# Performance work log

Hardware: AMD Instinct MI355X
Metric: run time of the kernel (lower is better)

The kernel has to match this reference:

```python
import jax, jax.numpy as jnp
import numpy as np

H = 32      # n_heads
KV = 8      # n_kv_heads
HD = 64     # head_dim = dim // n_heads


def setup_inputs() -> dict:
    key = jax.random.key(0)
    ks = jax.random.split(key, 8)
    B, S, D = 4, 1024, 2048
    x = jax.random.normal(ks[0], (B, S, D), dtype=jnp.float32)
    # RoPE tables stored as cos/sin parts of the complex freqs_cis (seqlen, head_dim//2)
    pos = jnp.arange(S, dtype=jnp.float32)[:, None]
    inv = 1.0 / (10000.0 ** (jnp.arange(0, HD, 2, dtype=jnp.float32) / HD))[None, :]
    ang = pos * inv                          # (S, HD//2)
    freqs_cos = jnp.cos(ang)
    freqs_sin = jnp.sin(ang)
    # additive causal mask (S, S): 0 on/below diagonal, -inf above
    mask = jnp.where(jnp.tril(jnp.ones((S, S), dtype=bool)), 0.0, -jnp.inf).astype(jnp.float32)
    sc = 0.02
    wq = jax.random.normal(ks[1], (H * HD, D), dtype=jnp.float32) * sc
    wk = jax.random.normal(ks[2], (KV * HD, D), dtype=jnp.float32) * sc
    wv = jax.random.normal(ks[3], (KV * HD, D), dtype=jnp.float32) * sc
    wo = jax.random.normal(ks[4], (D, D), dtype=jnp.float32) * sc
    return {"x": x, "freqs_cos": freqs_cos, "freqs_sin": freqs_sin, "mask": mask,
            "wq": wq, "wk": wk, "wv": wv, "wo": wo}


def _rope(t, cos, sin):
    # t: (B, S, nh, HD). Faithful to source: rotation is indexed by x.shape[2]
    # (the HEAD axis, due to pre-transpose call), broadcast over sequence.
    nh = t.shape[2]
    c = cos[:nh][None, None, :, :]           # (1,1,nh,HD//2)
    s = sin[:nh][None, None, :, :]
    tr = t.reshape(*t.shape[:-1], HD // 2, 2)
    t0, t1 = tr[..., 0], tr[..., 1]
    o0 = t0 * c - t1 * s
    o1 = t0 * s + t1 * c
    return jnp.stack([o0, o1], axis=-1).reshape(t.shape)


def reference(x, freqs_cos, freqs_sin, mask, wq, wk, wv, wo):
    B, S, D = x.shape
    xq = (x @ wq.T).reshape(B, S, H, HD)
    xk = (x @ wk.T).reshape(B, S, KV, HD)
    xv = (x @ wv.T).reshape(B, S, KV, HD)
    xq = _rope(xq, freqs_cos, freqs_sin)
    xk = _rope(xk, freqs_cos, freqs_sin)
    rep = H // KV
    xk = jnp.repeat(xk, rep, axis=2)         # GQA repeat_interleave on head axis
    xv = jnp.repeat(xv, rep, axis=2)
    q = xq.transpose(0, 2, 1, 3)             # (B,H,S,HD)
    k = xk.transpose(0, 2, 1, 3)
    v = xv.transpose(0, 2, 1, 3)
    scores = jnp.einsum('bhqd,bhkd->bhqk', q, k) / np.sqrt(HD).astype(np.float32)
    scores = scores + mask[None, None, :, :]
    p = jax.nn.softmax(scores.astype(jnp.float32), axis=-1).astype(q.dtype)
    out = jnp.einsum('bhqk,bhkd->bhqd', p, v)
    out = out.transpose(0, 2, 1, 3).reshape(B, S, H * HD)
    return out @ wo.T
```

## Files before the change

kernel.cpp:

```cpp
#include <hip/hip_runtime.h>
#include <hip/hip_bf16.h>

constexpr int kB  = 4;
constexpr int kS  = 1024;
constexpr int kD  = 2048;
constexpr int kH  = 32;
constexpr int kKV = 8;
constexpr int kHD = 64;
constexpr int kM  = kB * kS;
constexpr int kNT = kS / 64;

constexpr float kNegBig = -30000.0f;
constexpr float kC = 0.125f * 1.44269504f;
constexpr float kDeferThr = 40.0f;

typedef __attribute__((ext_vector_type(8))) short short8;
typedef __attribute__((ext_vector_type(4))) float floatx4;

static __device__ __forceinline__ short f2bf(float f) {
    unsigned int u = __builtin_bit_cast(unsigned int, f);
    unsigned int lsb = (u >> 16) & 1u;
    u += 0x7fffu + lsb;
    return (short)(u >> 16);
}
static __device__ __forceinline__ short f2bf_fast(float f) {
    unsigned int u = __builtin_bit_cast(unsigned int, f);
    return (short)((u + 0x8000u) >> 16);
}

static __device__ __forceinline__ void load_lds16(const short* g, short* l) {
    __builtin_amdgcn_global_load_lds(
        (const __attribute__((address_space(1))) unsigned int*)g,
        (__attribute__((address_space(3))) unsigned int*)l, 16, 0, 0);
}

__global__ void cast_f2b(const float* __restrict__ in, short* __restrict__ outp, int n4) {
    int gid = blockIdx.x * blockDim.x + threadIdx.x;
    if (gid >= n4) return;
    float4 v = ((const float4*)in)[gid];
    short4 o;
    o.x = f2bf(v.x); o.y = f2bf(v.y); o.z = f2bf(v.z); o.w = f2bf(v.w);
    ((short4*)outp)[gid] = o;
}

__global__ void cast4_f2b(const float* __restrict__ a, const float* __restrict__ b,
                          const float* __restrict__ c, const float* __restrict__ d,
                          short* __restrict__ oa, short* __restrict__ ob,
                          short* __restrict__ oc, short* __restrict__ od,
                          int na4, int nb4, int nc4, int nd4) {
    int gid = blockIdx.x * blockDim.x + threadIdx.x;
    const float* src; short* dst; int idx;
    if (gid < na4)                    { src = a; dst = oa; idx = gid; }
    else if (gid < na4 + nb4)         { src = b; dst = ob; idx = gid - na4; }
    else if (gid < na4 + nb4 + nc4)   { src = c; dst = oc; idx = gid - na4 - nb4; }
    else if (gid < na4+nb4+nc4+nd4)   { src = d; dst = od; idx = gid - na4 - nb4 - nc4; }
    else return;
    float4 v = ((const float4*)src)[idx];
    short4 o;
    o.x = f2bf(v.x); o.y = f2bf(v.y); o.z = f2bf(v.z); o.w = f2bf(v.w);
    ((short4*)dst)[idx] = o;
}

template <typename OT, int ROPE>
__global__ __launch_bounds__(256) void gemm_bt_lds(const short* __restrict__ A,
                                                   const short* __restrict__ Bm,
                                                   OT* __restrict__ C,
                                                   int M, int N, int K,
                                                   const float* __restrict__ cosb,
                                                   const float* __restrict__ sinb,
                                                   short* __restrict__ Vt,
                                                   const short* __restrict__ B2,
                                                   short* __restrict__ Kout) {
    __shared__ short As[128 * 32];
    __shared__ short Bs[128 * 32];

    int tid  = threadIdx.x;
    int wave = tid >> 6, lane = tid & 63;
    int quad = lane >> 4, l16 = lane & 15;
    int wm = wave >> 1, wn = wave & 1;

    int nwg  = gridDim.x * gridDim.y;
    int orig = blockIdx.y * gridDim.x + blockIdx.x;
    int wg   = orig;
    if ((nwg & 7) == 0) {
        int cpx = nwg >> 3;
        wg = (orig & 7) * cpx + (orig >> 3);
    }
    int bx = wg % gridDim.x, by = wg / gridDim.x;
    int m0 = by * 128, n0 = bx * 128;

    const short* Bblk;
    if constexpr (ROPE == 3)
        Bblk = (n0 < 2048) ? Bm + (long)n0 * K : B2 + (long)(n0 - 2048) * K;
    else
        Bblk = Bm + (long)n0 * K;

    floatx4 acc[4][4];
    for (int i = 0; i < 4; i++)
        for (int j = 0; j < 4; j++) acc[i][j] = (floatx4){0.f, 0.f, 0.f, 0.f};

    int srow = lane >> 2;
    int skc  = (lane & 3) * 8;

    for (int k0 = 0; k0 < K; k0 += 32) {
        __syncthreads();
        for (int i = 0; i < 2; i++) {
            int r16 = wave * 32 + i * 16;
            load_lds16(A + (long)(m0 + r16 + srow) * K + k0 + skc, &As[r16 * 32]);
            load_lds16(Bblk + (long)(r16 + srow) * K + k0 + skc, &Bs[r16 * 32]);
        }
        __syncthreads();

        short8 af[4], bfr[4];
        for (int i = 0; i < 4; i++)
            af[i] = *(const short8*)&As[(wm * 64 + i * 16 + l16) * 32 + quad * 8];
        for (int j = 0; j < 4; j++)
            bfr[j] = *(const short8*)&Bs[(wn * 64 + j * 16 + l16) * 32 + quad * 8];
        for (int i = 0; i < 4; i++)
            for (int j = 0; j < 4; j++)
                acc[i][j] = __builtin_amdgcn_mfma_f32_16x16x32_bf16(
                    af[i], bfr[j], acc[i][j], 0, 0, 0);
    }

    if constexpr (ROPE == 3) {
        for (int j = 0; j < 4; j++) {
            int col = n0 + wn * 64 + j * 16 + l16;
            if (col >= 2560) {
                int cv = col - 2560;
                for (int i = 0; i < 4; i++) {
                    int row0 = m0 + wm * 64 + i * 16 + quad * 4;
                    short4 o;
                    o.x = f2bf(acc[i][j][0]);
                    o.y = f2bf(acc[i][j][1]);
                    o.z = f2bf(acc[i][j][2]);
                    o.w = f2bf(acc[i][j][3]);
                    *(short4*)&Vt[(long)cv * M + row0] = o;
                }
            } else {
                bool isK = col >= 2048;
                int hh = isK ? ((col - 2048) >> 6) : (col >> 6);
                int ii = (col & 63) >> 1;
                float c = cosb[hh * 32 + ii];
                float s = sinb[hh * 32 + ii];
                for (int i = 0; i < 4; i++) {
                    for (int r = 0; r < 4; r++) {
                        int row = m0 + wm * 64 + i * 16 + quad * 4 + r;
                        float v = acc[i][j][r];
                        float p = __shfl_xor(v, 1);
                        v = (col & 1) ? (p * s + v * c)
                                      : (v * c - p * s);
                        if (isK)
                            Kout[(long)row * 1024 + (col - 2048)] = f2bf(v);
                        else
                            ((short*)C)[(long)row * 2048 + col] = f2bf(v);
                    }
                }
            }
        }
    } else {
        for (int j = 0; j < 4; j++) {
            int col = n0 + wn * 64 + j * 16 + l16;
            for (int i = 0; i < 4; i++)
                for (int r = 0; r < 4; r++) {
                    int row = m0 + wm * 64 + i * 16 + quad * 4 + r;
                    float v = acc[i][j][r];
                    if constexpr (sizeof(OT) == 2)
                        C[(long)row * N + col] = f2bf(v);
                    else
                        C[(long)row * N + col] = v;
                }
        }
    }
}

__global__ __launch_bounds__(256) void attn_kernel(const short* __restrict__ xq,
                                                   const short* __restrict__ xk,
                                                   const short* __restrict__ vt,
                                                   short* __restrict__ out,
                                                   int kvstride) {
    __shared__ short pT[4][32][72];

    int pb = blockIdx.x;
    int h = blockIdx.y, b = blockIdx.z;
    int kvh = h >> 2;
    int tid = threadIdx.x, wave = tid >> 6, lane = tid & 63;
    int quad = lane >> 4, l16 = lane & 15;

    const short* kbase0 = xk + (long)b * kS * kvstride + kvh * kHD;
    const short* vbase = vt + (long)kvh * kHD * kM + (long)b * kS;

    short8 ones;
    for (int i = 0; i < 8; i++) ones[i] = (short)0x3F80;

    auto loadK = [&](short8 (&kf)[4][2], int kt) {
        const short* kbase = kbase0 + (long)kt * 64 * kvstride;
#pragma unroll
        for (int kb = 0; kb < 4; kb++) {
            const short* kp = kbase + (long)(kb * 16 + l16) * kvstride + quad * 8;
            kf[kb][0] = *(const short8*)kp;
            kf[kb][1] = *(const short8*)(kp + 32);
        }
    };

    auto process = [&](int c) {
        int r0 = c * 128 + wave * 32;
        int nt = (r0 + 31) / 64 + 1;

        short8 qf[2][2];
#pragma unroll
        for (int g = 0; g < 2; g++) {
            const short* qp = xq + (((long)b * kS + r0 + g * 16 + l16) * kH + h) * kHD + quad * 8;
            qf[g][0] = *(const short8*)(qp);
            qf[g][1] = *(const short8*)(qp + 32);
        }

        float m_run[2][4];
        floatx4 acc_l[2];
        floatx4 acc_o[2][4];
#pragma unroll
        for (int g = 0; g < 2; g++) {
            acc_l[g] = (floatx4){0.f, 0.f, 0.f, 0.f};
            for (int r = 0; r < 4; r++) m_run[g][r] = kNegBig;
            for (int nb = 0; nb < 4; nb++) acc_o[g][nb] = (floatx4){0.f, 0.f, 0.f, 0.f};
        }

        short8 kf[4][2];
        loadK(kf, 0);

        for (int kt = 0; kt < nt; kt++) {
            short8 vf[4][2];
#pragma unroll
            for (int nb = 0; nb < 4; nb++) {
                const short* vp = vbase + (long)(nb * 16 + l16) * kM + kt * 64 + quad * 8;
                vf[nb][0] = *(const short8*)(vp);
                vf[nb][1] = *(const short8*)(vp + 32);
            }

            floatx4 accs[2][4];
            __builtin_amdgcn_s_setprio(1);
#pragma unroll
            for (int g = 0; g < 2; g++)
#pragma unroll
                for (int kb = 0; kb < 4; kb++) {
                    accs[g][kb] = (floatx4){0.f, 0.f, 0.f, 0.f};
                    accs[g][kb] = __builtin_amdgcn_mfma_f32_16x16x32_bf16(qf[g][0], kf[kb][0], accs[g][kb], 0, 0, 0);
                    accs[g][kb] = __builtin_amdgcn_mfma_f32_16x16x32_bf16(qf[g][1], kf[kb][1], accs[g][kb], 0, 0, 0);
                }
            __builtin_amdgcn_s_setprio(0);

            if (kt + 1 < nt) loadK(kf, kt + 1);

#pragma unroll
            for (int g = 0; g < 2; g++) {
                int wr0g = r0 + g * 16;
                if (kt * 64 + 63 > wr0g) {
                    int crow = wr0g + quad * 4;
#pragma unroll
                    for (int kb = 0; kb < 4; kb++)
#pragma unroll
                        for (int r = 0; r < 4; r++) {
                            int kj = kt * 64 + kb * 16 + l16;
                            if (kj > crow + r) accs[g][kb][r] = kNegBig;
                        }
                }
            }

#pragma unroll
            for (int g = 0; g < 2; g++) {
                float mx[4];
#pragma unroll
                for (int r = 0; r < 4; r++) {
                    float m1 = fmaxf(fmaxf(accs[g][0][r], accs[g][1][r]),
                                     fmaxf(accs[g][2][r], accs[g][3][r]));
                    for (int off = 1; off < 16; off <<= 1) m1 = fmaxf(m1, __shfl_xor(m1, off));
                    mx[r] = m1;
                }
                bool small = (mx[0] - m_run[g][0] <= kDeferThr) && (mx[1] - m_run[g][1] <= kDeferThr) &&
                             (mx[2] - m_run[g][2] <= kDeferThr) && (mx[3] - m_run[g][3] <= kDeferThr);
                if (!__all(small)) {
#pragma unroll
                    for (int r = 0; r < 4; r++) {
                        float mnew = fmaxf(m_run[g][r], mx[r]);
                        float alpha = exp2f((m_run[g][r] - mnew) * kC);
                        m_run[g][r] = mnew;
                        acc_l[g][r] *= alpha;
                        for (int nb = 0; nb < 4; nb++) acc_o[g][nb][r] *= alpha;
                    }
                }
#pragma unroll
                for (int r = 0; r < 4; r++) {
                    float mk = m_run[g][r] * kC;
                    for (int kb = 0; kb < 4; kb++)
                        accs[g][kb][r] = exp2f(fmaf(accs[g][kb][r], kC, -mk));
                }
            }

#pragma unroll
            for (int g = 0; g < 2; g++)
#pragma unroll
                for (int r = 0; r < 4; r++)
#pragma unroll
                    for (int kb = 0; kb < 4; kb++)
                        pT[wave][g * 16 + quad * 4 + r][kb * 16 + l16] = f2bf_fast(accs[g][kb][r]);

            __builtin_amdgcn_s_setprio(1);
#pragma unroll
            for (int g = 0; g < 2; g++) {
                short8 pf0 = *(const short8*)&pT[wave][g * 16 + l16][quad * 8];
                short8 pf1 = *(const short8*)&pT[wave][g * 16 + l16][32 + quad * 8];
                acc_l[g] = __builtin_amdgcn_mfma_f32_16x16x32_bf16(pf0, ones, acc_l[g], 0, 0, 0);
                acc_l[g] = __builtin_amdgcn_mfma_f32_16x16x32_bf16(pf1, ones, acc_l[g], 0, 0, 0);
#pragma unroll
                for (int nb = 0; nb < 4; nb++) {
                    acc_o[g][nb] = __builtin_amdgcn_mfma_f32_16x16x32_bf16(pf0, vf[nb][0], acc_o[g][nb], 0, 0, 0);
                    acc_o[g][nb] = __builtin_amdgcn_mfma_f32_16x16x32_bf16(pf1, vf[nb][1], acc_o[g][nb], 0, 0, 0);
                }
            }
            __builtin_amdgcn_s_setprio(0);
        }

#pragma unroll
        for (int g = 0; g < 2; g++)
#pragma unroll
            for (int r = 0; r < 4; r++) {
                float inv = 1.0f / fmaxf(acc_l[g][r], 1e-20f);
                int row = r0 + g * 16 + quad * 4 + r;
                for (int nb = 0; nb < 4; nb++)
                    out[(((long)b * kS + row) * kH + h) * kHD + nb * 16 + l16] =
                        f2bf(acc_o[g][nb][r] * inv);
            }
    };

    process(7 - pb);
    process(pb);
}

extern "C" void kernel_launch(void* const* d_in, const int* in_sizes, int n_in,
                              void* d_out, int out_size, void* d_ws, size_t ws_size,
                              hipStream_t stream) {
    const float* x  = (const float*)d_in[0];
    const float* fc = (const float*)d_in[1];
    const float* fs = (const float*)d_in[2];
    const float* wq = (const float*)d_in[4];
    const float* wk = (const float*)d_in[5];
    const float* wv = (const float*)d_in[6];
    const float* wo = (const float*)d_in[7];

    const int M = kM;
    const long MB = 1l << 20;

    char* ws = (char*)d_ws;
    short* xb   = (short*)(ws);
    short* wqb  = (short*)(ws + 16 * MB);
    short* ao   = (short*)(ws);
    short* wob  = (short*)(ws + 16 * MB);
    char*  dob  = (char*)d_out;
    short* xq   = (short*)(dob);
    short* xkv  = (short*)(dob + 16 * MB);
    short* vt   = (short*)(dob + 24 * MB);
    short* wkvb = (short*)(dob + 28 * MB);

    const int nX  = M * kD;
    const int nWq = kD * kD;
    const int nWk = kKV * kHD * kD;

    int total4 = (nX + nWq + 2 * nWk) / 4;
    cast4_f2b<<<(total4 + 255) / 256, 256, 0, stream>>>(
        x, wq, wk, wv, xb, wqb, wkvb, wkvb + nWk,
        nX / 4, nWq / 4, nWk / 4, nWk / 4);

    gemm_bt_lds<short, 3><<<dim3(3072 / 128, M / 128), 256, 0, stream>>>(
        xb, wqb, xq, M, 3072, kD, fc, fs, vt, wkvb, xkv);

    attn_kernel<<<dim3(4, kH, kB), 256, 0, stream>>>(
        xq, xkv, vt, ao, 1024);

    cast_f2b<<<(nWq / 4 + 255) / 256, 256, 0, stream>>>(wo, wob, nWq / 4);
    gemm_bt_lds<float, 0><<<dim3(kD / 128, M / 128), 256, 0, stream>>>(
        ao, wob, (float*)d_out, M, kD, kD, nullptr, nullptr, nullptr, nullptr, nullptr);
}
```

Measured before the change: 377.2 us.

## Double-buffer GEMM LDS tiles with XOR swizzle and MFMA priority boost

The GEMM main loop now double-buffers the A/B LDS tiles, issuing the next K-slice's global-to-LDS loads before computing on the current one. This leaves one barrier per iteration and is meant to overlap memory latency with MFMA work. It also XOR-swizzles the 16-byte column slots on both the load and read sides to cut LDS bank conflicts, and raises wave priority around the MFMA block. LDS use doubles, which may lower occupancy.

After: 352.9 us. 1.07x faster.

```diff
diff --git a/kernel.cpp b/kernel.cpp
--- a/kernel.cpp
+++ b/kernel.cpp
@@ -71,8 +71,8 @@
                                                    short* __restrict__ Vt,
                                                    const short* __restrict__ B2,
                                                    short* __restrict__ Kout) {
-    __shared__ short As[128 * 32];
-    __shared__ short Bs[128 * 32];
+    __shared__ short As[2 * 128 * 32];
+    __shared__ short Bs[2 * 128 * 32];
 
     int tid  = threadIdx.x;
     int wave = tid >> 6, lane = tid & 63;
@@ -99,27 +99,51 @@
     for (int i = 0; i < 4; i++)
         for (int j = 0; j < 4; j++) acc[i][j] = (floatx4){0.f, 0.f, 0.f, 0.f};
 
-    int srow = lane >> 2;
-    int skc  = (lane & 3) * 8;
-
-    for (int k0 = 0; k0 < K; k0 += 32) {
-        __syncthreads();
-        for (int i = 0; i < 2; i++) {
-            int r16 = wave * 32 + i * 16;
-            load_lds16(A + (long)(m0 + r16 + srow) * K + k0 + skc, &As[r16 * 32]);
-            load_lds16(Bblk + (long)(r16 + srow) * K + k0 + skc, &Bs[r16 * 32]);
-        }
-        __syncthreads();
+    int srow  = lane >> 2;
+    int sslot = (((lane & 3) ^ ((lane >> 3) & 3)) << 3);
+    int rsw   = ((l16 >> 1) & 3) << 3;
+    int rcol  = (quad * 8) ^ rsw;
+
+    const short* aP0 = A    + (long)(m0 + wave * 32 +      srow) * K + sslot;
+    const short* aP1 = A    + (long)(m0 + wave * 32 + 16 + srow) * K + sslot;
+    const short* bP0 = Bblk + (long)(     wave * 32 +      srow) * K + sslot;
+    const short* bP1 = Bblk + (long)(     wave * 32 + 16 + srow) * K + sslot;
+
+    auto stage = [&](int buf) {
+        int lb = buf * 4096 + (wave * 32) * 32;
+        load_lds16(aP0, &As[lb]);
+        load_lds16(aP1, &As[lb + 16 * 32]);
+        load_lds16(bP0, &Bs[lb]);
+        load_lds16(bP1, &Bs[lb + 16 * 32]);
+        aP0 += 32; aP1 += 32; bP0 += 32; bP1 += 32;
+    };
+
+    int nt = K >> 5;
+    stage(0);
+    __syncthreads();
+
+    for (int t = 0; t < nt; t++) {
+        int cur = t & 1;
+        if (t + 1 < nt) stage(cur ^ 1);
 
         short8 af[4], bfr[4];
+        int ab = cur * 4096;
+#pragma unroll
         for (int i = 0; i < 4; i++)
-            af[i] = *(const short8*)&As[(wm * 64 + i * 16 + l16) * 32 + quad * 8];
+            af[i] = *(const short8*)&As[ab + (wm * 64 + i * 16 + l16) * 32 + rcol];
+#pragma unroll
         for (int j = 0; j < 4; j++)
-            bfr[j] = *(const short8*)&Bs[(wn * 64 + j * 16 + l16) * 32 + quad * 8];
+            bfr[j] = *(const short8*)&Bs[ab + (wn * 64 + j * 16 + l16) * 32 + rcol];
+        __builtin_amdgcn_s_setprio(1);
+#pragma unroll
         for (int i = 0; i < 4; i++)
+#pragma unroll
             for (int j = 0; j < 4; j++)
                 acc[i][j] = __builtin_amdgcn_mfma_f32_16x16x32_bf16(
                     af[i], bfr[j], acc[i][j], 0, 0, 0);
+        __builtin_amdgcn_s_setprio(0);
+
+        __syncthreads();
     }
 
     if constexpr (ROPE == 3) {
```
